# Kernel optimization log

Hardware: AMD Instinct MI355X
Metric: run time of the kernel (lower is better)

Reference implementation:

```python
import jax, jax.numpy as jnp
import numpy as np


def _layernorm(x, g, b, eps=1e-5):
    m = x.mean(-1, keepdims=True)
    v = ((x - m) ** 2).mean(-1, keepdims=True)
    return (x - m) / jnp.sqrt(v + eps) * g + b


def _rel_pos_index(ws):
    # same construction as SwinWindowAttention.__init__
    coords = np.stack(np.meshgrid(np.arange(ws), np.arange(ws), indexing='ij')).reshape(2, -1)
    rel = (coords[:, :, None] - coords[:, None, :]).transpose(1, 2, 0).copy()
    rel[:, :, 0] += ws - 1
    rel[:, :, 1] += ws - 1
    rel[:, :, 0] *= 2 * ws - 1
    return jnp.asarray(rel.sum(-1))  # (N, N) int


def setup_inputs() -> dict:
    key = jax.random.key(0)
    ks = jax.random.split(key, 16)
    D, C, heads, ws = 2, 256, 8, 8
    B, H, W, Tq = 2, 128, 128, 512
    s = 0.02
    inp = {
        'x': jax.random.normal(ks[0], (B, H * W, C), jnp.float32),
        'query': jax.random.normal(ks[1], (Tq, B, C), jnp.float32),
        'blk_norm1_g': jnp.ones((D, C), jnp.float32),
        'blk_norm1_b': jnp.zeros((D, C), jnp.float32),
        'blk_qkv_w': jax.random.normal(ks[2], (D, 3 * C, C), jnp.float32) * s,
        'blk_qkv_b': jnp.zeros((D, 3 * C), jnp.float32),
        'blk_out_w': jax.random.normal(ks[3], (D, C, C), jnp.float32) * s,
        'blk_out_b': jnp.zeros((D, C), jnp.float32),
        'blk_rel_bias': jax.random.normal(ks[4], (D, (2 * ws - 1) ** 2, heads), jnp.float32) * s,
        'blk_norm2_g': jnp.ones((D, C), jnp.float32),
        'blk_norm2_b': jnp.zeros((D, C), jnp.float32),
        'blk_fc1_w': jax.random.normal(ks[5], (D, 4 * C, C), jnp.float32) * s,
        'blk_fc1_b': jnp.zeros((D, 4 * C), jnp.float32),
        'blk_fc2_w': jax.random.normal(ks[6], (D, C, 4 * C), jnp.float32) * s,
        'blk_fc2_b': jnp.zeros((D, C), jnp.float32),
        'ca_norm_g': jnp.ones((C,), jnp.float32),
        'ca_norm_b': jnp.zeros((C,), jnp.float32),
        'ca_projq_w': jax.random.normal(ks[7], (C, C), jnp.float32) * s,
        'ca_fc_w': jax.random.normal(ks[8], (C, C), jnp.float32) * s,
        'ca_fc_b': jnp.zeros((C,), jnp.float32),
        'ca_fc1_w': jax.random.normal(ks[9], (2 * C, C), jnp.float32) * s,
        'ca_fc1_b': jnp.zeros((2 * C,), jnp.float32),
        'ca_fc2_w': jax.random.normal(ks[10], (C, 2 * C), jnp.float32) * s,
        'ca_fc2_b': jnp.zeros((C,), jnp.float32),
        'H': H, 'W': W, 'window_size': ws, 'num_heads': heads,
    }
    return inp


def reference(x, query, blk_norm1_g, blk_norm1_b, blk_qkv_w, blk_qkv_b,
              blk_out_w, blk_out_b, blk_rel_bias, blk_norm2_g, blk_norm2_b,
              blk_fc1_w, blk_fc1_b, blk_fc2_w, blk_fc2_b,
              ca_norm_g, ca_norm_b, ca_projq_w, ca_fc_w, ca_fc_b,
              ca_fc1_w, ca_fc1_b, ca_fc2_w, ca_fc2_b,
              H, W, window_size, num_heads):
    B, L, C = x.shape
    ws = window_size
    hd = C // num_heads
    N = ws * ws
    rpi = _rel_pos_index(ws)  # (N, N) constant index map
    depth = blk_qkv_w.shape[0]

    for i in range(depth):
        # ---- windowed self-attention with relative position bias ----
        shortcut = x
        h = _layernorm(x, blk_norm1_g[i], blk_norm1_b[i])
        # window partition: (B,H,W,C) -> (B*nw, N, C)
        h = h.reshape(B, H // ws, ws, W // ws, ws, C)
        h = h.transpose(0, 1, 3, 2, 4, 5).reshape(-1, N, C)
        qkv = h @ blk_qkv_w[i].T + blk_qkv_b[i]  # (Bw, N, 3C)
        qkv = qkv.reshape(-1, N, 3, num_heads, hd).transpose(2, 0, 3, 1, 4)
        q, k, v = qkv[0], qkv[1], qkv[2]  # (Bw, h, N, d)
        attn = jnp.einsum('bhnd,bhmd->bhnm', q, k) * (hd ** -0.5)
        bias = blk_rel_bias[i][rpi]  # (N, N, h)
        attn = attn + bias.transpose(2, 0, 1)[None]
        attn = jax.nn.softmax(attn.astype(jnp.float32), axis=-1).astype(x.dtype)
        o = jnp.einsum('bhnm,bhmd->bhnd', attn, v)
        o = o.transpose(0, 2, 1, 3).reshape(-1, N, C)
        o = o @ blk_out_w[i].T + blk_out_b[i]
        # window reverse
        o = o.reshape(B, H // ws, W // ws, ws, ws, C)
        o = o.transpose(0, 1, 3, 2, 4, 5).reshape(B, H * W, C)
        x = shortcut + o
        # ---- MLP ----
        shortcut = x
        h = _layernorm(x, blk_norm2_g[i], blk_norm2_b[i])
        h = jax.nn.gelu(h @ blk_fc1_w[i].T + blk_fc1_b[i], approximate=False)
        h = h @ blk_fc2_w[i].T + blk_fc2_b[i]
        x = shortcut + h

    # ---- CrossAttnFFN: text query attends to image features ----
    kv = x.transpose(1, 0, 2)  # (Tk, B, C)
    Tq = query.shape[0]
    Tk = kv.shape[0]
    residual = query
    q = query @ ca_projq_w.T  # (Tq, B, C)
    qh = q.reshape(Tq, B, num_heads, hd).transpose(1, 2, 0, 3)   # (B,h,Tq,d)
    kh = kv.reshape(Tk, B, num_heads, hd).transpose(1, 2, 0, 3)  # (B,h,Tk,d)
    vh = kh
    attn = jnp.einsum('bhqd,bhkd->bhqk', qh, kh) / (hd ** 0.5)
    attn = jax.nn.softmax(attn.astype(jnp.float32), axis=-1).astype(query.dtype)
    ctx = jnp.einsum('bhqk,bhkd->bhqd', attn, vh)
    ctx = ctx.transpose(0, 2, 1, 3).reshape(B, Tq, C)
    ctx = ctx @ ca_fc_w.T + ca_fc_b
    ctx = jnp.clip(ctx, -32.0, 32.0)
    ctx = jax.nn.relu(ctx @ ca_fc1_w.T + ca_fc1_b)
    ctx = ctx @ ca_fc2_w.T + ca_fc2_b
    ctx = ctx.transpose(1, 0, 2)  # (Tq, B, C)
    out = _layernorm(residual + ctx, ca_norm_g, ca_norm_b)
    return out
```

## Files before the change

kernel.cpp:

```cpp
#include <hip/hip_runtime.h>
#include <hip/hip_bf16.h>


typedef unsigned short u16;
typedef u16  u16x4 __attribute__((ext_vector_type(4)));
typedef u16  u16x8 __attribute__((ext_vector_type(8)));
typedef short s16x8 __attribute__((ext_vector_type(8)));
typedef float f32x4 __attribute__((ext_vector_type(4)));
typedef unsigned int u32x4 __attribute__((ext_vector_type(4)));

#define LOG2E 1.4426950408889634f
#define SCALE_LOG2 0.25503480f

static __device__ __forceinline__ float bf2f(u16 u) {
    union { unsigned int i; float f; } v; v.i = ((unsigned int)u) << 16; return v.f;
}
static __device__ __forceinline__ u16 f2bf(float f) {
    unsigned int x = __float_as_uint(f);
    unsigned int r = x + 0x7fffu + ((x >> 16) & 1u);
    return (u16)(r >> 16);
}
static __device__ __forceinline__ unsigned int cvtpk(float a, float b) {
    unsigned int u;
    asm("v_cvt_pk_bf16_f32 %0, %1, %2" : "=v"(u) : "v"(a), "v"(b));
    return u;
}
static __device__ __forceinline__ void gld16(const u16* g, u16* l) {
    __builtin_amdgcn_global_load_lds(
        (const __attribute__((address_space(1))) unsigned int*)g,
        (__attribute__((address_space(3))) unsigned int*)l, 16, 0, 0);
}
#define EXP2F __builtin_amdgcn_exp2f

__launch_bounds__(256)
__global__ void cvt_weights(const float* __restrict__ qkvw, const float* __restrict__ outw,
                            const float* __restrict__ f1w,  const float* __restrict__ f2w,
                            const float* __restrict__ cpq,  const float* __restrict__ cfc,
                            const float* __restrict__ cf1,  const float* __restrict__ cf2,
                            const float* __restrict__ qry,  u16* __restrict__ dst) {
    const int q = blockIdx.x * 256 + threadIdx.x;
    const int gid = q * 4;
    const float* s; int off;
    if      (gid <  393216) { s = qkvw; off = 0;       }
    else if (gid <  524288) { s = outw; off = 393216;  }
    else if (gid < 1048576) { s = f1w;  off = 524288;  }
    else if (gid < 1572864) { s = f2w;  off = 1048576; }
    else if (gid < 1638400) { s = cpq;  off = 1572864; }
    else if (gid < 1703936) { s = cfc;  off = 1638400; }
    else if (gid < 1835008) { s = cf1;  off = 1703936; }
    else if (gid < 1966080) { s = cf2;  off = 1835008; }
    else                    { s = qry;  off = 1966080; }
    float4 v = *(const float4*)(s + (gid - off));
    u16x4 o; o[0] = f2bf(v.x); o[1] = f2bf(v.y); o[2] = f2bf(v.z); o[3] = f2bf(v.w);
    *(u16x4*)(dst + gid) = o;
}

__launch_bounds__(256)
__global__ void bias_frag_kernel(const float* __restrict__ rel, float* __restrict__ bfrag) {
    const int idx = blockIdx.x * 256 + threadIdx.x;
    #pragma unroll
    for (int j = 0; j < 4; ++j) {
        const int i = idx * 4 + j;
        const int layer = i >> 15, h = (i >> 12) & 7, kt = (i >> 10) & 3,
                  qt = (i >> 8) & 3, lane = (i >> 2) & 63, jj = i & 3;
        const int key   = (kt >> 1) * 32 + 4 * (kt & 1) + 8 * (lane >> 4) + jj;
        const int query = qt * 16 + (lane & 15);
        const int dy = (query >> 3) - (key >> 3) + 7;
        const int dx = (query & 7)  - (key & 7)  + 7;
        bfrag[i] = rel[layer * 1800 + (dy * 15 + dx) * 8 + h] * LOG2E;
    }
}

__launch_bounds__(256)
__global__ void ln_kernel(const float* __restrict__ in, u16* __restrict__ out,
                          const float* __restrict__ g, const float* __restrict__ b,
                          int rows) {
    const int wave = threadIdx.x >> 6, lane = threadIdx.x & 63;
    const int row = blockIdx.x * 4 + wave;
    if (row >= rows) return;
    const int c = lane * 4;
    float4 v = *(const float4*)(in + (size_t)row * 256 + c);
    float s1 = v.x + v.y + v.z + v.w;
    float s2 = v.x*v.x + v.y*v.y + v.z*v.z + v.w*v.w;
    #pragma unroll
    for (int off = 32; off; off >>= 1) {
        s1 += __shfl_xor(s1, off);
        s2 += __shfl_xor(s2, off);
    }
    const float mean = s1 * (1.f/256.f);
    const float var  = s2 * (1.f/256.f) - mean*mean;
    const float rstd = rsqrtf(var + 1e-5f);
    float4 gg = *(const float4*)(g + c);
    float4 bb = *(const float4*)(b + c);
    u16x4 og;
    og[0] = f2bf((v.x-mean)*rstd*gg.x + bb.x);
    og[1] = f2bf((v.y-mean)*rstd*gg.y + bb.y);
    og[2] = f2bf((v.z-mean)*rstd*gg.z + bb.z);
    og[3] = f2bf((v.w-mean)*rstd*gg.w + bb.w);
    *(u16x4*)(out + (size_t)row * 256 + c) = og;
}

template<int EPI, bool F32O>
__launch_bounds__(256)
__global__ void gemm128(const u16* __restrict__ A, const u16* __restrict__ W,
                        const float* __restrict__ bias, const float* __restrict__ resid,
                        void* __restrict__ outv, u16* __restrict__ aux,
                        int M, int N, int K) {
    __shared__ u16 As[128 * 64];
    __shared__ u16 Bs[128 * 64];
    const int nx = gridDim.x;
    const int nwg = nx * gridDim.y;
    int bid = blockIdx.y * nx + blockIdx.x;
    bid = (bid & 7) * (nwg >> 3) + (bid >> 3);
    const int m0 = (bid / nx) * 128, n0 = (bid % nx) * 128;
    const int tid = threadIdx.x, lane = tid & 63, wave = tid >> 6;
    const int g = lane >> 4, c = lane & 15;
    const int wm = (wave >> 1) * 64, wn = (wave & 1) * 64;

    f32x4 acc[4][4];
    #pragma unroll
    for (int i = 0; i < 4; ++i)
        #pragma unroll
        for (int j = 0; j < 4; ++j) acc[i][j] = f32x4{0.f,0.f,0.f,0.f};

    const int srow = (lane >> 3);
    const int scol = ((lane & 7) ^ srow) * 8;
    const int cx = c & 7;
    for (int k0 = 0; k0 < K; k0 += 64) {
        #pragma unroll
        for (int i = 0; i < 4; ++i) {
            const int ch = wave * 4 + i;
            const int r = ch * 8 + srow;
            gld16(&A[(size_t)(m0 + r) * K + k0 + scol], &As[ch * 512]);
            gld16(&W[(size_t)(n0 + r) * K + k0 + scol], &Bs[ch * 512]);
        }
        __syncthreads();
        #pragma unroll
        for (int kk = 0; kk < 64; kk += 32) {
            const int slot = (kk >> 3) + g;
            s16x8 af[4], bf_[4];
            #pragma unroll
            for (int mi = 0; mi < 4; ++mi)
                af[mi] = *(const s16x8*)&As[(wm + mi*16 + c) * 64 + (slot ^ cx) * 8];
            #pragma unroll
            for (int ni = 0; ni < 4; ++ni)
                bf_[ni] = *(const s16x8*)&Bs[(wn + ni*16 + c) * 64 + (slot ^ cx) * 8];
            #pragma unroll
            for (int mi = 0; mi < 4; ++mi)
                #pragma unroll
                for (int ni = 0; ni < 4; ++ni)
                    acc[mi][ni] = __builtin_amdgcn_mfma_f32_16x16x32_bf16(
                        af[mi], bf_[ni], acc[mi][ni], 0, 0, 0);
        }
        __syncthreads();
    }

    #pragma unroll
    for (int mi = 0; mi < 4; ++mi) {
        #pragma unroll
        for (int ni = 0; ni < 4; ++ni) {
            const int col = n0 + wn + ni*16 + c;
            if (EPI == 7 && col >= 512) {
                const int row0 = m0 + wm + mi*16 + g*4;
                const int bidx = row0 >> 14, y = (row0 >> 7) & 127, xx0 = row0 & 127;
                const int wini = (bidx*16 + (y>>3))*16 + (xx0>>3);
                const int key0 = ((y&7)<<3) | (xx0&7);
                const float bb2 = bias[col];
                u16x4 pv;
                #pragma unroll
                for (int j = 0; j < 4; ++j) pv[j] = f2bf(acc[mi][ni][j] + bb2);
                *(u16x4*)&aux[((size_t)wini*256 + (col-512))*64 + key0] = pv;
                continue;
            }
            #pragma unroll
            for (int j = 0; j < 4; ++j) {
                const int row = m0 + wm + mi*16 + g*4 + j;
                float v = acc[mi][ni][j];
                v += bias[col];
                if (EPI == 2) {
                    const float t = EXP2F(2.3022082f * fmaf(0.044715f * v, v * v, v));
                    v = v * t * __builtin_amdgcn_rcpf(t + 1.f);
                }
                if (EPI == 3 || EPI == 8) v += resid[(size_t)row * N + col];
                if (EPI == 8) {
                    ((float*)outv)[(size_t)row * N + col] = v;
                    aux[(size_t)row * N + col] = f2bf(v);
                    continue;
                }
                if (EPI == 7 && col < 256) v *= SCALE_LOG2;
                if (F32O) ((float*)outv)[(size_t)row * N + col] = v;
                else      ((u16*)outv)[(size_t)row * N + col]   = f2bf(v);
            }
        }
    }
}

template<int EPI>
__launch_bounds__(256)
__global__ void gemm_bt(const u16* __restrict__ A, const u16* __restrict__ W,
                        const float* __restrict__ bias, u16* __restrict__ out,
                        int M, int N, int K) {
    __shared__ u16 As[64][72];
    __shared__ u16 Bs[64][72];
    const int m0 = blockIdx.y * 64;
    const int n0 = blockIdx.x * 64;
    const int tid = threadIdx.x;
    const int lane = tid & 63, wave = tid >> 6;
    const int wm = (wave >> 1) * 32, wn = (wave & 1) * 32;

    f32x4 acc[2][2];
    #pragma unroll
    for (int i = 0; i < 2; ++i)
        #pragma unroll
        for (int j = 0; j < 2; ++j) acc[i][j] = f32x4{0.f,0.f,0.f,0.f};

    for (int k0 = 0; k0 < K; k0 += 64) {
        #pragma unroll
        for (int rep = 0; rep < 2; ++rep) {
            int i = tid + rep * 256;
            int r = i >> 3, c = (i & 7) * 8;
            *(s16x8*)&As[r][c] = *(const s16x8*)&A[(size_t)(m0 + r) * K + k0 + c];
            *(s16x8*)&Bs[r][c] = *(const s16x8*)&W[(size_t)(n0 + r) * K + k0 + c];
        }
        __syncthreads();
        #pragma unroll
        for (int kk = 0; kk < 64; kk += 32) {
            s16x8 af[2], bfr[2];
            #pragma unroll
            for (int i = 0; i < 2; ++i) {
                af[i]  = *(const s16x8*)&As[wm + i*16 + (lane & 15)][kk + (lane >> 4) * 8];
                bfr[i] = *(const s16x8*)&Bs[wn + i*16 + (lane & 15)][kk + (lane >> 4) * 8];
            }
            #pragma unroll
            for (int mi = 0; mi < 2; ++mi)
                #pragma unroll
                for (int ni = 0; ni < 2; ++ni)
                    acc[mi][ni] = __builtin_amdgcn_mfma_f32_16x16x32_bf16(
                        af[mi], bfr[ni], acc[mi][ni], 0, 0, 0);
        }
        __syncthreads();
    }

    #pragma unroll
    for (int mi = 0; mi < 2; ++mi) {
        #pragma unroll
        for (int ni = 0; ni < 2; ++ni) {
            const int col = n0 + wn + ni*16 + (lane & 15);
            #pragma unroll
            for (int j = 0; j < 4; ++j) {
                const int row = m0 + wm + mi*16 + (lane >> 4)*4 + j;
                float v = acc[mi][ni][j];
                if (EPI >= 1 && EPI <= 5) v += bias[col];
                if (EPI == 4) v = fmaxf(v, 0.f);
                if (EPI == 5) v = fminf(fmaxf(v, -32.f), 32.f);
                if (EPI == 6) v *= SCALE_LOG2;
                out[(size_t)row * N + col] = f2bf(v);
            }
        }
    }
}

__launch_bounds__(256)
__global__ void win_attn(const u16* __restrict__ qkv, const u16* __restrict__ vtbuf,
                         const float* __restrict__ bfrag, u16* __restrict__ o,
                         int layer) {
    const int wid = blockIdx.x * 4 + (threadIdx.x >> 6);
    const int lane = threadIdx.x & 63;
    const int h = wid & 7, win = wid >> 3;
    const int b = win >> 8, wy = (win >> 4) & 15, wx = win & 15;
    const int g = lane >> 4, c = lane & 15;
    const size_t rowbase = (size_t)b * 16384 + (size_t)wy * 8 * 128 + wx * 8;

    s16x8 qf[4], kf[4];
    #pragma unroll
    for (int qt = 0; qt < 4; ++qt) {
        const int t = qt * 16 + c;
        qf[qt] = *(const s16x8*)&qkv[(rowbase + (size_t)(t >> 3) * 128 + (t & 7)) * 768
                                     + h * 32 + g * 8];
    }
    const int kp0 = 8 * (c >> 2) + (c & 3);
    #pragma unroll
    for (int kt = 0; kt < 4; ++kt) {
        const int t = (kt >> 1) * 32 + 4 * (kt & 1) + kp0;
        kf[kt] = *(const s16x8*)&qkv[(rowbase + (size_t)(t >> 3) * 128 + (t & 7)) * 768
                                     + 256 + h * 32 + g * 8];
    }

    const float* bb = bfrag + (size_t)((layer * 8 + h) * 16) * 256;
    f32x4 st[4][4];
    #pragma unroll
    for (int kt = 0; kt < 4; ++kt)
        #pragma unroll
        for (int qt = 0; qt < 4; ++qt)
            st[kt][qt] = *(const f32x4*)&bb[(kt * 4 + qt) * 256 + lane * 4];
    #pragma unroll
    for (int kt = 0; kt < 4; ++kt)
        #pragma unroll
        for (int qt = 0; qt < 4; ++qt)
            st[kt][qt] = __builtin_amdgcn_mfma_f32_16x16x32_bf16(
                kf[kt], qf[qt], st[kt][qt], 0, 0, 0);

    float linv[4];
    #pragma unroll
    for (int qt = 0; qt < 4; ++qt) {
        float sum = 0.f;
        #pragma unroll
        for (int kt = 0; kt < 4; ++kt)
            #pragma unroll
            for (int j = 0; j < 4; ++j) {
                const float p = EXP2F(st[kt][qt][j]);
                st[kt][qt][j] = p;
                sum += p;
            }
        sum += __shfl_xor(sum, 16);
        sum += __shfl_xor(sum, 32);
        linv[qt] = 1.f / sum;
    }

    const u16* vb = vtbuf + ((size_t)win * 256 + h * 32) * 64;
    s16x8 vf[2][2];
    #pragma unroll
    for (int dt = 0; dt < 2; ++dt)
        #pragma unroll
        for (int ks = 0; ks < 2; ++ks)
            vf[dt][ks] = *(const s16x8*)&vb[(size_t)(dt * 16 + c) * 64 + ks * 32 + g * 8];

    f32x4 acc[4][2];
    #pragma unroll
    for (int i = 0; i < 4; ++i)
        #pragma unroll
        for (int j = 0; j < 2; ++j) acc[i][j] = f32x4{0.f,0.f,0.f,0.f};

    #pragma unroll
    for (int qt = 0; qt < 4; ++qt) {
        #pragma unroll
        for (int ks = 0; ks < 2; ++ks) {
            u32x4 w;
            w[0] = cvtpk(st[2*ks][qt][0],   st[2*ks][qt][1]);
            w[1] = cvtpk(st[2*ks][qt][2],   st[2*ks][qt][3]);
            w[2] = cvtpk(st[2*ks+1][qt][0], st[2*ks+1][qt][1]);
            w[3] = cvtpk(st[2*ks+1][qt][2], st[2*ks+1][qt][3]);
            const s16x8 pfrag = __builtin_bit_cast(s16x8, w);
            acc[qt][0] = __builtin_amdgcn_mfma_f32_16x16x32_bf16(pfrag, vf[0][ks], acc[qt][0], 0,0,0);
            acc[qt][1] = __builtin_amdgcn_mfma_f32_16x16x32_bf16(pfrag, vf[1][ks], acc[qt][1], 0,0,0);
        }
    }

    #pragma unroll
    for (int qt = 0; qt < 4; ++qt)
        #pragma unroll
        for (int dt = 0; dt < 2; ++dt)
            #pragma unroll
            for (int j = 0; j < 4; ++j) {
                const int t = qt * 16 + g * 4 + j;
                o[(rowbase + (size_t)(t >> 3) * 128 + (t & 7)) * 256
                  + h * 32 + dt * 16 + c] = f2bf(acc[qt][dt][j] * linv[qt]);
            }
}

__launch_bounds__(256)
__global__ void tr_kernel(const u16* __restrict__ src, u16* __restrict__ dst) {
    __shared__ u16 T[64][72];
    const int b = blockIdx.z;
    const int n0 = blockIdx.x * 64, c0 = blockIdx.y * 64;
    const int r = threadIdx.x >> 3, cc = (threadIdx.x & 7) * 8;
    const u16* S = src + (size_t)b * 16384 * 256;
    u16* D = dst + (size_t)b * 256 * 16384;
    #pragma unroll
    for (int rr = 0; rr < 64; rr += 32)
        *(u16x8*)&T[r + rr][cc] = *(const u16x8*)&S[(size_t)(n0 + r + rr) * 256 + c0 + cc];
    __syncthreads();
    #pragma unroll
    for (int rr = 0; rr < 64; rr += 32) {
        u16x8 v;
        #pragma unroll
        for (int k2 = 0; k2 < 8; ++k2) v[k2] = T[cc + k2][r + rr];
        *(u16x8*)&D[(size_t)(c0 + r + rr) * 16384 + n0 + cc] = v;
    }
}

__launch_bounds__(256)
__global__ void ca_flash(const u16* __restrict__ qb, const u16* __restrict__ xb,
                         const u16* __restrict__ xbT, float* __restrict__ pbuf) {
    const int wid = blockIdx.x * 4 + (threadIdx.x >> 6);
    const int lane = threadIdx.x & 63;
    const int ks = wid & 31, qt = (wid >> 5) & 3, h = (wid >> 7) & 7, b = wid >> 10;
    const int g = lane >> 4, c = lane & 15;
    const int kp0 = 8 * (c >> 2) + (c & 3);

    s16x8 qf[8];
    #pragma unroll
    for (int nt = 0; nt < 8; ++nt) {
        const int q = qt * 128 + nt * 16 + c;
        qf[nt] = *(const s16x8*)&qb[((size_t)q * 2 + b) * 256 + h * 32 + g * 8];
    }
    const u16* Kb = xb  + (size_t)b * 16384 * 256 + h * 32;
    const u16* Vb = xbT + (size_t)b * 256 * 16384 + (size_t)(h * 32) * 16384;

    s16x8 ones;
    #pragma unroll
    for (int j = 0; j < 8; ++j) ones[j] = (short)0x3F80;

    f32x4 acc[2][8];
    f32x4 accl[8];
    #pragma unroll
    for (int j = 0; j < 8; ++j) {
        acc[0][j] = f32x4{0.f,0.f,0.f,0.f};
        acc[1][j] = f32x4{0.f,0.f,0.f,0.f};
        accl[j]   = f32x4{0.f,0.f,0.f,0.f};
    }

    const int base = ks * 512;
    const f32x4 zero = f32x4{0.f, 0.f, 0.f, 0.f};
    for (int step = 0; step < 16; ++step) {
        const int n0 = base + step * 32;
        const s16x8 kf0 = *(const s16x8*)&Kb[(size_t)(n0 + kp0) * 256 + g * 8];
        const s16x8 kf1 = *(const s16x8*)&Kb[(size_t)(n0 + kp0 + 4) * 256 + g * 8];
        const s16x8 vf0 = *(const s16x8*)&Vb[(size_t)c * 16384 + n0 + g * 8];
        const s16x8 vf1 = *(const s16x8*)&Vb[(size_t)(16 + c) * 16384 + n0 + g * 8];
        #pragma unroll
        for (int nt = 0; nt < 8; ++nt) {
            const f32x4 sa = __builtin_amdgcn_mfma_f32_16x16x32_bf16(kf0, qf[nt], zero, 0, 0, 0);
            const f32x4 sb = __builtin_amdgcn_mfma_f32_16x16x32_bf16(kf1, qf[nt], zero, 0, 0, 0);
            u32x4 w;
            w[0] = cvtpk(EXP2F(sa[0]), EXP2F(sa[1]));
            w[1] = cvtpk(EXP2F(sa[2]), EXP2F(sa[3]));
            w[2] = cvtpk(EXP2F(sb[0]), EXP2F(sb[1]));
            w[3] = cvtpk(EXP2F(sb[2]), EXP2F(sb[3]));
            const s16x8 pf = __builtin_bit_cast(s16x8, w);
            acc[0][nt] = __builtin_amdgcn_mfma_f32_16x16x32_bf16(vf0, pf, acc[0][nt], 0, 0, 0);
            acc[1][nt] = __builtin_amdgcn_mfma_f32_16x16x32_bf16(vf1, pf, acc[1][nt], 0, 0, 0);
            accl[nt]   = __builtin_amdgcn_mfma_f32_16x16x32_bf16(ones, pf, accl[nt], 0, 0, 0);
        }
    }

    float* P = pbuf + (size_t)wid * 4224;
    if (g == 0) {
        #pragma unroll
        for (int nt = 0; nt < 8; ++nt)
            P[nt * 16 + c] = accl[nt][0];
    }
    #pragma unroll
    for (int mi = 0; mi < 2; ++mi)
        #pragma unroll
        for (int nt = 0; nt < 8; ++nt)
            *(f32x4*)&P[128 + (c + 16*nt) * 32 + 16*mi + g*4] = acc[mi][nt];
}

__launch_bounds__(256)
__global__ void ca_merge(const float* __restrict__ pbuf, u16* __restrict__ ctx) {
    const int wave = threadIdx.x >> 6, lane = threadIdx.x & 63;
    const int sub = lane >> 5, d = lane & 31;
    const int rowid = blockIdx.x * 8 + wave * 2 + sub;
    const int t = rowid & 511, h = (rowid >> 9) & 7, b = rowid >> 12;
    const int qt = t >> 7, qq = t & 127;
    const size_t w0 = (size_t)((b * 8 + h) * 4 + qt) * 32;
    float L = 0.f, o = 0.f;
    #pragma unroll
    for (int i = 0; i < 32; ++i) {
        L += pbuf[(w0 + i) * 4224 + qq];
        o += pbuf[(w0 + i) * 4224 + 128 + qq * 32 + d];
    }
    ctx[((size_t)b * 512 + t) * 256 + h * 32 + d] = f2bf(o / L);
}

__launch_bounds__(256)
__global__ void final_ln(const float* __restrict__ query, const u16* __restrict__ ctx4,
                         const float* __restrict__ g, const float* __restrict__ b,
                         float* __restrict__ out) {
    const int wave = threadIdx.x >> 6, lane = threadIdx.x & 63;
    const int row = blockIdx.x * 4 + wave;
    const int t = row >> 1, bb = row & 1;
    const int c = lane * 4;
    float4 rq = *(const float4*)(query + (size_t)row * 256 + c);
    u16x4 rc = *(const u16x4*)(ctx4 + ((size_t)bb * 512 + t) * 256 + c);
    float x0 = rq.x + bf2f(rc[0]);
    float x1 = rq.y + bf2f(rc[1]);
    float x2 = rq.z + bf2f(rc[2]);
    float x3 = rq.w + bf2f(rc[3]);
    float s1 = x0 + x1 + x2 + x3;
    float s2 = x0*x0 + x1*x1 + x2*x2 + x3*x3;
    #pragma unroll
    for (int off = 32; off; off >>= 1) {
        s1 += __shfl_xor(s1, off);
        s2 += __shfl_xor(s2, off);
    }
    const float mean = s1 * (1.f/256.f);
    const float var  = s2 * (1.f/256.f) - mean*mean;
    const float rstd = rsqrtf(var + 1e-5f);
    float4 gg = *(const float4*)(g + c);
    float4 bv = *(const float4*)(b + c);
    float4 og;
    og.x = (x0-mean)*rstd*gg.x + bv.x;
    og.y = (x1-mean)*rstd*gg.y + bv.y;
    og.z = (x2-mean)*rstd*gg.z + bv.z;
    og.w = (x3-mean)*rstd*gg.w + bv.w;
    *(float4*)(out + (size_t)row * 256 + c) = og;
}


extern "C" void kernel_launch(void* const* d_in, const int* in_sizes, int n_in,
                              void* d_out, int out_size, void* d_ws, size_t ws_size,
                              hipStream_t stream) {
    const float* x_in  = (const float*)d_in[0];
    const float* query = (const float*)d_in[1];
    const float* n1_g  = (const float*)d_in[2];
    const float* n1_b  = (const float*)d_in[3];
    const float* qkv_w = (const float*)d_in[4];
    const float* qkv_b = (const float*)d_in[5];
    const float* out_w = (const float*)d_in[6];
    const float* out_b = (const float*)d_in[7];
    const float* rel   = (const float*)d_in[8];
    const float* n2_g  = (const float*)d_in[9];
    const float* n2_b  = (const float*)d_in[10];
    const float* fc1_w = (const float*)d_in[11];
    const float* fc1_b = (const float*)d_in[12];
    const float* fc2_w = (const float*)d_in[13];
    const float* fc2_b = (const float*)d_in[14];
    const float* can_g = (const float*)d_in[15];
    const float* can_b = (const float*)d_in[16];
    const float* cpq_w = (const float*)d_in[17];
    const float* cfc_w = (const float*)d_in[18];
    const float* cfc_b = (const float*)d_in[19];
    const float* cf1_w = (const float*)d_in[20];
    const float* cf1_b = (const float*)d_in[21];
    const float* cf2_w = (const float*)d_in[22];
    const float* cf2_b = (const float*)d_in[23];

    const int M = 32768;

    char* w = (char*)d_ws;
    float* xs  = (float*)w;  w += (size_t)M * 256 * 4;
    u16* hbuf  = (u16*)w;    w += (size_t)M * 256 * 2;
    u16* big   = (u16*)w;    w += (size_t)M * 1024 * 2;
    u16* arena = (u16*)w;    w += (size_t)2228224 * 2;
    u16* qbuf  = (u16*)w;    w += 524288;
    u16* ctx1  = (u16*)w;    w += 524288;
    u16* ctx2  = (u16*)w;    w += 524288;
    u16* ctx3  = (u16*)w;    w += 1048576;
    u16* ctx4  = (u16*)w;    w += 524288;
    u16* xb    = (u16*)w;    w += (size_t)M * 256 * 2;
    float* bfragb = (float*)w; w += 65536 * 4;

    u16* vtbuf = big + (size_t)M * 768;
    u16*   xbT  = big;
    float* pbuf = (float*)(big + 8388608);

    u16* wq   = arena;
    u16* wo   = arena + 393216;
    u16* wf1  = arena + 524288;
    u16* wf2  = arena + 1048576;
    u16* wcpq = arena + 1572864;
    u16* wcfc = arena + 1638400;
    u16* wcf1 = arena + 1703936;
    u16* wcf2 = arena + 1835008;
    u16* qcvt = arena + 1966080;

    cvt_weights<<<2176, 256, 0, stream>>>(qkv_w, out_w, fc1_w, fc2_w, cpq_w,
                                          cfc_w, cf1_w, cf2_w, query, arena);
    bias_frag_kernel<<<64, 256, 0, stream>>>(rel, bfragb);

    for (int i = 0; i < 2; ++i) {
        const float* src = (i == 0) ? x_in : xs;
        ln_kernel<<<M/4, 256, 0, stream>>>(src, hbuf, n1_g + i*256, n1_b + i*256, M);
        gemm128<7,false><<<dim3(6,256), 256, 0, stream>>>(
            hbuf, wq + (size_t)i*768*256, qkv_b + i*768, nullptr, big, vtbuf, M, 768, 256);
        win_attn<<<1024, 256, 0, stream>>>(big, vtbuf, bfragb, hbuf, i);
        gemm128<3,true><<<dim3(2,256), 256, 0, stream>>>(
            hbuf, wo + (size_t)i*65536, out_b + i*256, src, xs, nullptr, M, 256, 256);
        ln_kernel<<<M/4, 256, 0, stream>>>(xs, hbuf, n2_g + i*256, n2_b + i*256, M);
        gemm128<2,false><<<dim3(8,256), 256, 0, stream>>>(
            hbuf, wf1 + (size_t)i*262144, fc1_b + i*1024, nullptr, big, nullptr, M, 1024, 256);
        if (i == 0)
            gemm128<3,true><<<dim3(2,256), 256, 0, stream>>>(
                big, wf2, fc2_b, xs, xs, nullptr, M, 256, 1024);
        else
            gemm128<8,true><<<dim3(2,256), 256, 0, stream>>>(
                big, wf2 + 262144, fc2_b + 256, xs, xs, xb, M, 256, 1024);
    }

    tr_kernel<<<dim3(256, 4, 2), 256, 0, stream>>>(xb, xbT);
    gemm_bt<6><<<dim3(4, 16), 256, 0, stream>>>(qcvt, wcpq, nullptr, qbuf, 1024, 256, 256);
    ca_flash<<<512, 256, 0, stream>>>(qbuf, xb, xbT, pbuf);
    ca_merge<<<1024, 256, 0, stream>>>(pbuf, ctx1);
    gemm_bt<5><<<dim3(4, 16), 256, 0, stream>>>(ctx1, wcfc, cfc_b, ctx2, 1024, 256, 256);
    gemm_bt<4><<<dim3(8, 16), 256, 0, stream>>>(ctx2, wcf1, cf1_b, ctx3, 1024, 512, 256);
    gemm_bt<1><<<dim3(4, 16), 256, 0, stream>>>(ctx3, wcf2, cf2_b, ctx4, 1024, 256, 512);
    final_ln<<<256, 256, 0, stream>>>(query, ctx4, can_g, can_b, (float*)d_out);

    (void)in_sizes; (void)n_in; (void)out_size; (void)ws_size;
}
```

Before: 402.2 us.

## Fuse residual GEMMs with following LayerNorm and split cross-attn keys finer

Adds a full-row (N=256) GEMM kernel that applies bias and residual, then computes the following LayerNorm in its epilogue, writing both the fp32 residual stream and the bf16 normalized input. This removes three separate ln_kernel passes that would otherwise re-read the residual stream. Separately, the cross-attention flash kernel now splits keys into 64 chunks instead of 32, doubling the wave count, and stores the partial outputs in bf16 to shrink merge traffic. The risks are lower occupancy in the big fused tile (512 threads, large LDS), a one-pass variance computation, and bf16 rounding of the unnormalized partial sums.

```diff
diff --git a/kernel.cpp b/kernel.cpp
--- a/kernel.cpp
+++ b/kernel.cpp
@@ -181,8 +181,8 @@
                     const float t = EXP2F(2.3022082f * fmaf(0.044715f * v, v * v, v));
                     v = v * t * __builtin_amdgcn_rcpf(t + 1.f);
                 }
-                if (EPI == 3 || EPI == 8) v += resid[(size_t)row * N + col];
                 if (EPI == 8) {
+                    v += resid[(size_t)row * N + col];
                     ((float*)outv)[(size_t)row * N + col] = v;
                     aux[(size_t)row * N + col] = f2bf(v);
                     continue;
@@ -193,6 +193,127 @@
             }
         }
     }
+}
+
+__launch_bounds__(512)
+__global__ void gemm_n256_ln(const u16* __restrict__ A, const u16* __restrict__ W,
+                             const float* __restrict__ bias, const float* __restrict__ resid,
+                             const float* __restrict__ lng, const float* __restrict__ lnb,
+                             float* __restrict__ xs_out, u16* __restrict__ hb_out, int K) {
+    __shared__ u16 As[128 * 64];
+    __shared__ u16 Bs[256 * 64];
+    __shared__ float red[128][8];
+    const int nwg = gridDim.x;
+    int bid = blockIdx.x;
+    bid = (bid & 7) * (nwg >> 3) + (bid >> 3);
+    const int m0 = bid * 128;
+    const int tid = threadIdx.x, lane = tid & 63, w = tid >> 6;
+    const int g = lane >> 4, c = lane & 15;
+    const int wr = w >> 2, wc = w & 3;
+
+    f32x4 acc[4][4];
+    #pragma unroll
+    for (int i = 0; i < 4; ++i)
+        #pragma unroll
+        for (int j = 0; j < 4; ++j) acc[i][j] = f32x4{0.f,0.f,0.f,0.f};
+
+    const int srow = lane >> 3;
+    const int scol = ((lane & 7) ^ srow) * 8;
+    const int cx = c & 7;
+    for (int k0 = 0; k0 < K; k0 += 64) {
+        #pragma unroll
+        for (int r = 0; r < 2; ++r) {
+            const int ch = w + r * 8;
+            gld16(&A[(size_t)(m0 + ch * 8 + srow) * K + k0 + scol], &As[ch * 512]);
+        }
+        #pragma unroll
+        for (int r = 0; r < 4; ++r) {
+            const int ch = w + r * 8;
+            gld16(&W[(size_t)(ch * 8 + srow) * K + k0 + scol], &Bs[ch * 512]);
+        }
+        __syncthreads();
+        #pragma unroll
+        for (int kk = 0; kk < 64; kk += 32) {
+            const int slot = (kk >> 3) + g;
+            s16x8 af[4], bf_[4];
+            #pragma unroll
+            for (int mi = 0; mi < 4; ++mi)
+                af[mi] = *(const s16x8*)&As[(wr*64 + mi*16 + c) * 64 + (slot ^ cx) * 8];
+            #pragma unroll
+            for (int ni = 0; ni < 4; ++ni)
+                bf_[ni] = *(const s16x8*)&Bs[(wc*64 + ni*16 + c) * 64 + (slot ^ cx) * 8];
+            #pragma unroll
+            for (int mi = 0; mi < 4; ++mi)
+                #pragma unroll
+                for (int ni = 0; ni < 4; ++ni)
+                    acc[mi][ni] = __builtin_amdgcn_mfma_f32_16x16x32_bf16(
+                        af[mi], bf_[ni], acc[mi][ni], 0, 0, 0);
+        }
+        __syncthreads();
+    }
+
+    #pragma unroll
+    for (int mi = 0; mi < 4; ++mi)
+        #pragma unroll
+        for (int ni = 0; ni < 4; ++ni) {
+            const int col = wc*64 + ni*16 + c;
+            const float bb = bias[col];
+            #pragma unroll
+            for (int j = 0; j < 4; ++j) {
+                const int row = m0 + wr*64 + mi*16 + g*4 + j;
+                acc[mi][ni][j] += bb + resid[(size_t)row * 256 + col];
+            }
+        }
+
+    #pragma unroll
+    for (int mi = 0; mi < 4; ++mi)
+        #pragma unroll
+        for (int j = 0; j < 4; ++j) {
+            float a  = acc[mi][0][j] + acc[mi][1][j] + acc[mi][2][j] + acc[mi][3][j];
+            float b2 = acc[mi][0][j]*acc[mi][0][j] + acc[mi][1][j]*acc[mi][1][j]
+                     + acc[mi][2][j]*acc[mi][2][j] + acc[mi][3][j]*acc[mi][3][j];
+            #pragma unroll
+            for (int off = 1; off < 16; off <<= 1) {
+                a  += __shfl_xor(a, off);
+                b2 += __shfl_xor(b2, off);
+            }
+            if (c == 0) {
+                const int rl = wr*64 + mi*16 + g*4 + j;
+                red[rl][wc*2]     = a;
+                red[rl][wc*2 + 1] = b2;
+            }
+        }
+    __syncthreads();
+
+    float mean_[4][4], rstd_[4][4];
+    #pragma unroll
+    for (int mi = 0; mi < 4; ++mi)
+        #pragma unroll
+        for (int j = 0; j < 4; ++j) {
+            const int rl = wr*64 + mi*16 + g*4 + j;
+            const float s1 = red[rl][0] + red[rl][2] + red[rl][4] + red[rl][6];
+            const float s2 = red[rl][1] + red[rl][3] + red[rl][5] + red[rl][7];
+            const float mn = s1 * (1.f/256.f);
+            const float vr = s2 * (1.f/256.f) - mn*mn;
+            mean_[mi][j] = mn;
+            rstd_[mi][j] = rsqrtf(vr + 1e-5f);
+        }
+
+    #pragma unroll
+    for (int mi = 0; mi < 4; ++mi)
+        #pragma unroll
+        for (int ni = 0; ni < 4; ++ni) {
+            const int col = wc*64 + ni*16 + c;
+            const float gc = lng[col], bc = lnb[col];
+            #pragma unroll
+            for (int j = 0; j < 4; ++j) {
+                const int row = m0 + wr*64 + mi*16 + g*4 + j;
+                const float v = acc[mi][ni][j];
+                xs_out[(size_t)row * 256 + col] = v;
+                hb_out[(size_t)row * 256 + col] =
+                    f2bf((v - mean_[mi][j]) * rstd_[mi][j] * gc + bc);
+            }
+        }
 }
 
 template<int EPI>
@@ -381,10 +502,11 @@
 
 __launch_bounds__(256)
 __global__ void ca_flash(const u16* __restrict__ qb, const u16* __restrict__ xb,
-                         const u16* __restrict__ xbT, float* __restrict__ pbuf) {
+                         const u16* __restrict__ xbT, float* __restrict__ pl,
+                         u16* __restrict__ pO) {
     const int wid = blockIdx.x * 4 + (threadIdx.x >> 6);
     const int lane = threadIdx.x & 63;
-    const int ks = wid & 31, qt = (wid >> 5) & 3, h = (wid >> 7) & 7, b = wid >> 10;
+    const int ks = wid & 63, qt = (wid >> 6) & 3, h = (wid >> 8) & 7, b = wid >> 11;
     const int g = lane >> 4, c = lane & 15;
     const int kp0 = 8 * (c >> 2) + (c & 3);
 
@@ -410,9 +532,9 @@
         accl[j]   = f32x4{0.f,0.f,0.f,0.f};
     }
 
-    const int base = ks * 512;
+    const int base = ks * 256;
     const f32x4 zero = f32x4{0.f, 0.f, 0.f, 0.f};
-    for (int step = 0; step < 16; ++step) {
+    for (int step = 0; step < 8; ++step) {
         const int n0 = base + step * 32;
         const s16x8 kf0 = *(const s16x8*)&Kb[(size_t)(n0 + kp0) * 256 + g * 8];
         const s16x8 kf1 = *(const s16x8*)&Kb[(size_t)(n0 + kp0 + 4) * 256 + g * 8];
@@ -434,32 +556,39 @@
         }
     }
 
-    float* P = pbuf + (size_t)wid * 4224;
+    float* Pl = pl + (size_t)wid * 128;
+    u16*   Po = pO + (size_t)wid * 4096;
     if (g == 0) {
         #pragma unroll
         for (int nt = 0; nt < 8; ++nt)
-            P[nt * 16 + c] = accl[nt][0];
+            Pl[nt * 16 + c] = accl[nt][0];
     }
     #pragma unroll
     for (int mi = 0; mi < 2; ++mi)
         #pragma unroll
-        for (int nt = 0; nt < 8; ++nt)
-            *(f32x4*)&P[128 + (c + 16*nt) * 32 + 16*mi + g*4] = acc[mi][nt];
-}
-
-__launch_bounds__(256)
-__global__ void ca_merge(const float* __restrict__ pbuf, u16* __restrict__ ctx) {
+        for (int nt = 0; nt < 8; ++nt) {
+            const unsigned int w0_ = cvtpk(acc[mi][nt][0], acc[mi][nt][1]);
+            const unsigned int w1_ = cvtpk(acc[mi][nt][2], acc[mi][nt][3]);
+            u16* dst = &Po[(size_t)(c + 16*nt) * 32 + 16*mi + g*4];
+            *(unsigned int*)dst       = w0_;
+            *(unsigned int*)(dst + 2) = w1_;
+        }
+}
+
+__launch_bounds__(256)
+__global__ void ca_merge(const float* __restrict__ pl, const u16* __restrict__ pO,
+                         u16* __restrict__ ctx) {
     const int wave = threadIdx.x >> 6, lane = threadIdx.x & 63;
     const int sub = lane >> 5, d = lane & 31;
     const int rowid = blockIdx.x * 8 + wave * 2 + sub;
     const int t = rowid & 511, h = (rowid >> 9) & 7, b = rowid >> 12;
     const int qt = t >> 7, qq = t & 127;
-    const size_t w0 = (size_t)((b * 8 + h) * 4 + qt) * 32;
+    const size_t w0 = (size_t)((b * 8 + h) * 4 + qt) * 64;
     float L = 0.f, o = 0.f;
     #pragma unroll
-    for (int i = 0; i < 32; ++i) {
-        L += pbuf[(w0 + i) * 4224 + qq];
-        o += pbuf[(w0 + i) * 4224 + 128 + qq * 32 + d];
+    for (int i = 0; i < 64; ++i) {
+        L += pl[(w0 + i) * 128 + qq];
+        o += bf2f(pO[((w0 + i) * 128 + qq) * 32 + d]);
     }
     ctx[((size_t)b * 512 + t) * 256 + h * 32 + d] = f2bf(o / L);
 }
@@ -544,7 +673,8 @@
 
     u16* vtbuf = big + (size_t)M * 768;
     u16*   xbT  = big;
-    float* pbuf = (float*)(big + 8388608);
+    float* pbl = (float*)(big + 8388608);
+    u16*   pbO = (u16*)(pbl + 4096 * 128);
 
     u16* wq   = arena;
     u16* wo   = arena + 393216;
@@ -560,29 +690,31 @@
                                           cfc_w, cf1_w, cf2_w, query, arena);
     bias_frag_kernel<<<64, 256, 0, stream>>>(rel, bfragb);
 
-    for (int i = 0; i < 2; ++i) {
-        const float* src = (i == 0) ? x_in : xs;
-        ln_kernel<<<M/4, 256, 0, stream>>>(src, hbuf, n1_g + i*256, n1_b + i*256, M);
-        gemm128<7,false><<<dim3(6,256), 256, 0, stream>>>(
-            hbuf, wq + (size_t)i*768*256, qkv_b + i*768, nullptr, big, vtbuf, M, 768, 256);
-        win_attn<<<1024, 256, 0, stream>>>(big, vtbuf, bfragb, hbuf, i);
-        gemm128<3,true><<<dim3(2,256), 256, 0, stream>>>(
-            hbuf, wo + (size_t)i*65536, out_b + i*256, src, xs, nullptr, M, 256, 256);
-        ln_kernel<<<M/4, 256, 0, stream>>>(xs, hbuf, n2_g + i*256, n2_b + i*256, M);
-        gemm128<2,false><<<dim3(8,256), 256, 0, stream>>>(
-            hbuf, wf1 + (size_t)i*262144, fc1_b + i*1024, nullptr, big, nullptr, M, 1024, 256);
-        if (i == 0)
-            gemm128<3,true><<<dim3(2,256), 256, 0, stream>>>(
-                big, wf2, fc2_b, xs, xs, nullptr, M, 256, 1024);
-        else
-            gemm128<8,true><<<dim3(2,256), 256, 0, stream>>>(
-                big, wf2 + 262144, fc2_b + 256, xs, xs, xb, M, 256, 1024);
-    }
+    ln_kernel<<<M/4, 256, 0, stream>>>(x_in, hbuf, n1_g, n1_b, M);
+    gemm128<7,false><<<dim3(6,256), 256, 0, stream>>>(
+        hbuf, wq, qkv_b, nullptr, big, vtbuf, M, 768, 256);
+    win_attn<<<1024, 256, 0, stream>>>(big, vtbuf, bfragb, hbuf, 0);
+    gemm_n256_ln<<<256, 512, 0, stream>>>(
+        hbuf, wo, out_b, x_in, n2_g, n2_b, xs, hbuf, 256);
+    gemm128<2,false><<<dim3(8,256), 256, 0, stream>>>(
+        hbuf, wf1, fc1_b, nullptr, big, nullptr, M, 1024, 256);
+    gemm_n256_ln<<<256, 512, 0, stream>>>(
+        big, wf2, fc2_b, xs, n1_g + 256, n1_b + 256, xs, hbuf, 1024);
+
+    gemm128<7,false><<<dim3(6,256), 256, 0, stream>>>(
+        hbuf, wq + (size_t)768*256, qkv_b + 768, nullptr, big, vtbuf, M, 768, 256);
+    win_attn<<<1024, 256, 0, stream>>>(big, vtbuf, bfragb, hbuf, 1);
+    gemm_n256_ln<<<256, 512, 0, stream>>>(
+        hbuf, wo + 65536, out_b + 256, xs, n2_g + 256, n2_b + 256, xs, hbuf, 256);
+    gemm128<2,false><<<dim3(8,256), 256, 0, stream>>>(
+        hbuf, wf1 + 262144, fc1_b + 1024, nullptr, big, nullptr, M, 1024, 256);
+    gemm128<8,true><<<dim3(2,256), 256, 0, stream>>>(
+        big, wf2 + 262144, fc2_b + 256, xs, xs, xb, M, 256, 1024);
 
     tr_kernel<<<dim3(256, 4, 2), 256, 0, stream>>>(xb, xbT);
     gemm_bt<6><<<dim3(4, 16), 256, 0, stream>>>(qcvt, wcpq, nullptr, qbuf, 1024, 256, 256);
-    ca_flash<<<512, 256, 0, stream>>>(qbuf, xb, xbT, pbuf);
-    ca_merge<<<1024, 256, 0, stream>>>(pbuf, ctx1);
+    ca_flash<<<1024, 256, 0, stream>>>(qbuf, xb, xbT, pbl, pbO);
+    ca_merge<<<1024, 256, 0, stream>>>(pbl, pbO, ctx1);
     gemm_bt<5><<<dim3(4, 16), 256, 0, stream>>>(ctx1, wcfc, cfc_b, ctx2, 1024, 256, 256);
     gemm_bt<4><<<dim3(8, 16), 256, 0, stream>>>(ctx2, wcf1, cf1_b, ctx3, 1024, 512, 256);
     gemm_bt<1><<<dim3(4, 16), 256, 0, stream>>>(ctx3, wcf2, cf2_b, ctx4, 1024, 256, 512);
```

Measured after the change: 414.4 us. +3.0%, slower.
